# Performance work log

Hardware: AMD Instinct MI355X
Metric: run time of the kernel (lower is better)

## Reference

```python
import jax, jax.numpy as jnp
import numpy as np

B, C_ATT, C_VAL = 1, 64, 64
T, H, W = 40, 32, 32
HW = H * W
TOPK = 10
TEMP = 0.07
NEIGHBOR_RANGE = 24  # circle mode -> radius = 24 // 2
NON_MASK_LEN = 1     # first frame is not masked
NEG_INF = -1e30


def _spatial_neighbor_circle(h, w, neighbor_range):
    """Circle-mode spatial neighbor mask, (h*w, h*w) bool."""
    radius = neighbor_range // 2
    gy, gx = jnp.meshgrid(jnp.arange(h, dtype=jnp.float32),
                          jnp.arange(w, dtype=jnp.float32), indexing='ij')
    dy = gy[:, :, None, None] - gy[None, None, :, :]
    dx = gx[:, :, None, None] - gx[None, None, :, :]
    dist = jnp.sqrt(dy * dy + dx * dx)
    return (dist < radius).reshape(h * w, h * w)


def setup_inputs() -> dict:
    key0 = jax.random.key(0)
    k1, k2, k3 = jax.random.split(key0, 3)
    query = jax.random.normal(k1, (B, C_ATT, H, W), dtype=jnp.float32)
    key = jax.random.normal(k2, (B, C_ATT, T, H, W), dtype=jnp.float32)
    value = jax.random.normal(k3, (B, C_VAL, T, H, W), dtype=jnp.float32)
    mask = _spatial_neighbor_circle(H, W, NEIGHBOR_RANGE)  # (HW, HW) bool
    return {"query": query, "key": key, "value": value, "mask": mask}


def _l2_normalize(x, axis, eps=1e-12):
    # matches F.normalize(p=2): x / max(||x||, eps)
    n = jnp.sqrt(jnp.sum(x * x, axis=axis, keepdims=True))
    return x / jnp.maximum(n, eps)


def reference(query, key, value, mask):
    # normalize along channel dim
    q = _l2_normalize(query, axis=1).reshape(B, C_ATT, HW)          # (B,C,Q)
    k = _l2_normalize(key, axis=1).reshape(B, C_ATT, T * HW)        # (B,C,K)
    v = value.reshape(B, C_VAL, T * HW)                             # (B,Cv,K)

    # affinity over all keys vs all queries (chunking in the original is a
    # pure memory optimization; the math per query column is identical)
    aff = jnp.einsum('bck,bcq->bkq', k, q) / TEMP                   # (B,K,Q)

    # build full mask: first NON_MASK_LEN frames fully visible, remaining
    # frames restricted to the spatial-neighbor circle
    tiled = jnp.tile(mask, (T - NON_MASK_LEN, 1))                   # ((T-nm)*HW, Q)
    full_mask = jnp.concatenate(
        [jnp.ones((NON_MASK_LEN * HW, HW), dtype=bool), tiled], axis=0)  # (K,Q)
    aff = jnp.where(full_mask[None], aff, NEG_INF)

    # top-k over the key dimension, per query
    aff_qk = jnp.swapaxes(aff, 1, 2)                                # (B,Q,K)
    top_vals, top_idx = jax.lax.top_k(aff_qk, TOPK)                 # (B,Q,topk)
    weights = jax.nn.softmax(top_vals, axis=-1)                     # (B,Q,topk)

    # gather top-k values: (B,Cv,Q,topk)
    gathered = jnp.take_along_axis(v[:, :, None, :], top_idx[:, None, :, :], axis=3)
    out = jnp.einsum('bcqk,bqk->bcq', gathered, weights)            # (B,Cv,Q)
    return out.reshape(B, C_VAL, H, W)
```

## Files before the change

kernel.cpp:

```cpp
#include <hip/hip_runtime.h>
#include <hip/hip_bf16.h>
#include <float.h>

#define HWQ   1024
#define NK    40960
#define NCH   64
#define NTOP  10
#define NF0JOB 8
#define PVLEN (NF0JOB * NTOP)
#define CAPG  384
#define CAPW  16
#define R2    144
#define TOTU  23556
#define NBLK  1024
#define TSCALE 14.2857142857142857f
#define LOSCL  4.8828125e-4f

typedef _Float16 f16x8 __attribute__((ext_vector_type(8)));
typedef float    f32x4 __attribute__((ext_vector_type(4)));
typedef unsigned short us8 __attribute__((ext_vector_type(8)));
typedef unsigned long long u64;
typedef unsigned int       u32;

__device__ inline float bf16bits_to_f32(unsigned short u) {
    union { u32 i; float f; } z; z.i = ((u32)u) << 16; return z.f;
}
__device__ inline unsigned short f32_to_bf16bits(float x) {
    __hip_bfloat16 b = __float2bfloat16(x);
    return *(unsigned short*)&b;
}

__device__ inline int sniff_fp32(const unsigned short* __restrict__ raw) {
    const int lane = threadIdx.x & 63;
    const int e = (raw[lane] >> 7) & 0xFF;
    const u64 m = __ballot(e < 100 || e > 133);
    return __popcll(m) > 16;
}

__device__ inline u32 ord32(float v) {
    const u32 b = __float_as_uint(v);
    return b ^ (u32)(((int)b >> 31) | (int)0x80000000);
}
__device__ inline u64 pack_vi(float val, int kidx) {
    return ((u64)ord32(val) << 16) | (u32)(0xFFFF - kidx);
}
__device__ inline float unpack_val(u64 p) {
    const u32 u = (u32)(p >> 16);
    const u32 b = u ^ (~((u32)((int)u >> 31)) | 0x80000000u);
    return __uint_as_float(b);
}
__device__ inline int unpack_idx(u64 p) { return 0xFFFF - (int)(p & 0xFFFF); }

__device__ inline void ins10(u64* v, u64 pk) {
#pragma unroll
    for (int j = NTOP - 1; j >= 1; --j) {
        const bool gj = pk > v[j];
        const bool gp = pk > v[j - 1];
        v[j] = gj ? (gp ? v[j - 1] : pk) : v[j];
    }
    if (pk > v[0]) v[0] = pk;
}

__global__ __launch_bounds__(256) void prep_all(
    const void* __restrict__ qin_, const void* __restrict__ kin_,
    const void* __restrict__ vin_,
    f16x8* __restrict__ kh, f16x8* __restrict__ kl,
    f16x8* __restrict__ qh, f16x8* __restrict__ ql,
    unsigned short* __restrict__ vt, int* __restrict__ cnt)
{
    __shared__ float ssq[4][64];
    const int isf  = sniff_fp32((const unsigned short*)kin_);
    const int bid  = blockIdx.x;
    const int tid  = threadIdx.x;
    const int w    = tid >> 6;
    const int lane = tid & 63;
    const int c0   = w * 16;

    if (bid == 655) {
        cnt[tid * 4 + 0] = 0; cnt[tid * 4 + 1] = 0;
        cnt[tid * 4 + 2] = 0; cnt[tid * 4 + 3] = 0;
    }

    if (bid < 640) {
        const int key = bid * 64 + lane;
        float x[16];
        if (isf) {
            const float* p = (const float*)kin_;
#pragma unroll
            for (int i = 0; i < 16; ++i) x[i] = p[(c0 + i) * NK + key];
        } else {
            const __hip_bfloat16* p = (const __hip_bfloat16*)kin_;
#pragma unroll
            for (int i = 0; i < 16; ++i) x[i] = __bfloat162float(p[(c0 + i) * NK + key]);
        }
        float s = 0.f;
#pragma unroll
        for (int i = 0; i < 16; ++i) s = fmaf(x[i], x[i], s);
        ssq[w][lane] = s;
        __syncthreads();
        s = ssq[0][lane] + ssq[1][lane] + ssq[2][lane] + ssq[3][lane];
        const float rn = 1.0f / fmaxf(sqrtf(s), 1e-12f);

        const int tb = (key >> 4) * 128 + (key & 15);
#pragma unroll
        for (int b2 = 0; b2 < 2; ++b2) {
            f16x8 h, l;
#pragma unroll
            for (int jj = 0; jj < 8; ++jj) {
                const float xv = x[b2 * 8 + jj] * rn;
                const _Float16 hh = (_Float16)xv;
                h[jj] = hh;
                l[jj] = (_Float16)((xv - (float)hh) * 2048.0f);
            }
            kh[tb + (w * 2 + b2) * 16] = h;
            kl[tb + (w * 2 + b2) * 16] = l;
        }

        unsigned short vv[16];
        if (isf) {
            const float* p = (const float*)vin_;
#pragma unroll
            for (int i = 0; i < 16; ++i) vv[i] = f32_to_bf16bits(p[(c0 + i) * NK + key]);
        } else {
            const unsigned short* p = (const unsigned short*)vin_;
#pragma unroll
            for (int i = 0; i < 16; ++i) vv[i] = p[(c0 + i) * NK + key];
        }
        us8* dst = (us8*)(vt + (size_t)key * NCH + c0);
#pragma unroll
        for (int b2 = 0; b2 < 2; ++b2) {
            us8 o;
#pragma unroll
            for (int e = 0; e < 8; ++e) o[e] = vv[b2 * 8 + e];
            dst[b2] = o;
        }
    } else {
        const int q = (bid - 640) * 64 + lane;
        float x[16];
        if (isf) {
            const float* p = (const float*)qin_;
#pragma unroll
            for (int i = 0; i < 16; ++i) x[i] = p[(c0 + i) * HWQ + q];
        } else {
            const __hip_bfloat16* p = (const __hip_bfloat16*)qin_;
#pragma unroll
            for (int i = 0; i < 16; ++i) x[i] = __bfloat162float(p[(c0 + i) * HWQ + q]);
        }
        float s = 0.f;
#pragma unroll
        for (int i = 0; i < 16; ++i) s = fmaf(x[i], x[i], s);
        ssq[w][lane] = s;
        __syncthreads();
        s = ssq[0][lane] + ssq[1][lane] + ssq[2][lane] + ssq[3][lane];
        const float rn = 1.0f / fmaxf(sqrtf(s), 1e-12f);

        const int tb = (q >> 4) * 128 + (q & 15);
#pragma unroll
        for (int b2 = 0; b2 < 2; ++b2) {
            f16x8 h, l;
#pragma unroll
            for (int jj = 0; jj < 8; ++jj) {
                const float xv = x[b2 * 8 + jj] * rn;
                const _Float16 hh = (_Float16)xv;
                h[jj] = hh;
                l[jj] = (_Float16)((xv - (float)hh) * 2048.0f);
            }
            qh[tb + (w * 2 + b2) * 16] = h;
            ql[tb + (w * 2 + b2) * 16] = l;
        }
    }
}

__device__ inline void quad_merge_store(
    u64 (*sm)[16][NTOP], int lane, u64* out10)
{
    int p0 = 0, p1 = 0, p2 = 0, p3 = 0;
#pragma unroll
    for (int r = 0; r < NTOP; ++r) {
        const u64 h0 = sm[0][lane][p0], h1 = sm[1][lane][p1];
        const u64 h2 = sm[2][lane][p2], h3 = sm[3][lane][p3];
        u64 m = h0; int sel = 0;
        if (h1 > m) { m = h1; sel = 1; }
        if (h2 > m) { m = h2; sel = 2; }
        if (h3 > m) { m = h3; sel = 3; }
        out10[r] = m;
        p0 += (sel == 0); p1 += (sel == 1); p2 += (sel == 2); p3 += (sel == 3);
    }
}

__global__ __launch_bounds__(128) void attn_f0(
    const f16x8* __restrict__ kh, const f16x8* __restrict__ kl,
    const f16x8* __restrict__ qh, const f16x8* __restrict__ ql,
    u64* __restrict__ pv)
{
    __shared__ u64 sm[2][4][16][NTOP];

    const int tid  = threadIdx.x;
    const int w    = tid >> 6;
    const int lane = tid & 63;
    const int quad = lane >> 4;
    const int n    = lane & 15;

    const int t   = blockIdx.x * 2 + w;
    const int job = blockIdx.y;

    const int qb = t * 128 + n;
    const f16x8 bh0 = qh[qb + quad * 16];
    const f16x8 bh1 = qh[qb + (4 + quad) * 16];
    const f16x8 bl0 = ql[qb + quad * 16];
    const f16x8 bl1 = ql[qb + (4 + quad) * 16];

    u64 v[NTOP];
#pragma unroll
    for (int jj = 0; jj < NTOP; ++jj) v[jj] = 0ull;

    const int start = job * 8, end = start + 8;
    const int loff = (n + quad * 16) * 16;
    const char* ph = (const char*)kh + (size_t)start * 2048 + loff;
    const char* pl = (const char*)kl + (size_t)start * 2048 + loff;

    for (int kt = start; kt < end; ++kt) {
        const f16x8 Ah0 = *(const f16x8*)(ph);
        const f16x8 Ah1 = *(const f16x8*)(ph + 1024);
        const f16x8 Al0 = *(const f16x8*)(pl);
        const f16x8 Al1 = *(const f16x8*)(pl + 1024);

        f32x4 accH = {0.f,0.f,0.f,0.f}, accL0 = {0.f,0.f,0.f,0.f}, accL1 = {0.f,0.f,0.f,0.f};
        accH  = __builtin_amdgcn_mfma_f32_16x16x32_f16(Ah0, bh0, accH, 0, 0, 0);
        accH  = __builtin_amdgcn_mfma_f32_16x16x32_f16(Ah1, bh1, accH, 0, 0, 0);
        accL0 = __builtin_amdgcn_mfma_f32_16x16x32_f16(Ah0, bl0, accL0, 0, 0, 0);
        accL0 = __builtin_amdgcn_mfma_f32_16x16x32_f16(Al0, bh0, accL0, 0, 0, 0);
        accL1 = __builtin_amdgcn_mfma_f32_16x16x32_f16(Ah1, bl1, accL1, 0, 0, 0);
        accL1 = __builtin_amdgcn_mfma_f32_16x16x32_f16(Al1, bh1, accL1, 0, 0, 0);

        const int key0 = kt * 16 + quad * 4;
#pragma unroll
        for (int r = 0; r < 4; ++r) {
            const float val = fmaf(accL0[r] + accL1[r], LOSCL, accH[r]);
            const u64 pk = pack_vi(val, key0 + r);
            if (pk > v[NTOP - 1]) ins10(v, pk);
        }
        ph += 2048; pl += 2048;
    }

#pragma unroll
    for (int jj = 0; jj < NTOP; ++jj) sm[w][quad][n][jj] = v[jj];
    __syncthreads();

    if (lane < 16) {
        u64 out10[NTOP];
        quad_merge_store(sm[w], lane, out10);
        const int q = t * 16 + lane;
#pragma unroll
        for (int r = 0; r < NTOP; ++r) pv[(size_t)q * PVLEN + job * NTOP + r] = out10[r];
    }
}

__global__ __launch_bounds__(256) void theta_refine(
    const u64* __restrict__ pv, float* __restrict__ thmax)
{
    const int q    = blockIdx.x * 4 + (threadIdx.x >> 6);
    const int lane = threadIdx.x & 63;

    u64 l0 = pv[(size_t)q * PVLEN + lane];
    u64 l1 = (lane < 16) ? pv[(size_t)q * PVLEN + 64 + lane] : 0ull;

    u64 m = 0ull;
#pragma unroll
    for (int r = 0; r < NTOP; ++r) {
        u64 c = l0 > l1 ? l0 : l1;
#pragma unroll
        for (int off = 32; off >= 1; off >>= 1) {
            const u32 lo = (u32)c, hi = (u32)(c >> 32);
            const u32 lo2 = (u32)__shfl_xor((int)lo, off);
            const u32 hi2 = (u32)__shfl_xor((int)hi, off);
            const u64 o = ((u64)hi2 << 32) | lo2;
            if (o > c) c = o;
        }
        if (l0 == c) l0 = 0ull;
        if (l1 == c) l1 = 0ull;
        m = c;
    }
    if (lane == 0) thmax[q] = unpack_val(m);
}

__global__ __launch_bounds__(256, 4) void attn_masked(
    const f16x8* __restrict__ kh, const f16x8* __restrict__ kl,
    const f16x8* __restrict__ qh, const f16x8* __restrict__ ql,
    const float* __restrict__ thmax,
    u64* __restrict__ gcand, int* __restrict__ cnt)
{
    __shared__ u64 wcand[4][32][CAPW];
    __shared__ int wcnt[4][32];

    const int tid  = threadIdx.x;
    const int w    = tid >> 6;
    const int lane = tid & 63;
    const int quad = lane >> 4;
    const int n    = lane & 15;

    if (lane < 32) wcnt[w][lane] = 0;

    const int bidx = ((int)blockIdx.x & 7) * (NBLK / 8) + ((int)blockIdx.x >> 3);
    const int wid  = bidx * 4 + w;
    const int u0   = (int)(((long long)wid * TOTU) >> 12);
    const int u1   = (int)(((long long)(wid + 1) * TOTU) >> 12);

    f16x8 b0h0, b0h1, b0l0, b0l1, b1h0, b1h1, b1l0, b1l1;
    float theta0 = 0.f, theta1 = 0.f;
    int cur_qy = -1, q0 = 0;

    for (int u = u0; u < u1; ++u) {
        const int fm1 = u / 604;
        const int rem = u - fm1 * 604;
        int qy, off;
        if (rem < 210) {
            int t = (int)((sqrtf((float)(529 + 8 * rem)) - 23.0f) * 0.5f);
            while ((t * (t + 23)) / 2 > rem) --t;
            while (((t + 1) * (t + 24)) / 2 <= rem) ++t;
            qy = t; off = rem - (t * (t + 23)) / 2;
        } else if (rem < 417) {
            qy = 12 + (rem - 210) / 23; off = (rem - 210) % 23;
        } else {
            const int s = 603 - rem;
            int t = (int)((sqrtf((float)(529 + 8 * s)) - 23.0f) * 0.5f);
            while ((t * (t + 23)) / 2 > s) --t;
            while (((t + 1) * (t + 24)) / 2 <= s) ++t;
            qy = 31 - t;
            off = (12 + t) - 1 - (s - (t * (t + 23)) / 2);
        }
        const int rlo = (qy > 11) ? qy - 11 : 0;
        const int row = rlo + off;
        const int frame = fm1 + 1;

        if (qy != cur_qy) {
            if (cur_qy >= 0) {
                __builtin_amdgcn_wave_barrier();
                if (lane < 32) {
                    const int rc = min(wcnt[w][lane], CAPW);
                    if (rc > 0) {
                        const int qq = cur_qy * 32 + lane;
                        const int base = atomicAdd(&cnt[qq], rc);
                        for (int jf = 0; jf < rc; ++jf) {
                            const int pos = base + jf;
                            if (pos < CAPG) gcand[(size_t)qq * CAPG + pos] = wcand[w][lane][jf];
                        }
                    }
                    wcnt[w][lane] = 0;
                }
                __builtin_amdgcn_wave_barrier();
            }
            cur_qy = qy;
            const int qb = qy * 256 + n;
            b0h0 = qh[qb + quad * 16];       b0h1 = qh[qb + (4 + quad) * 16];
            b0l0 = ql[qb + quad * 16];       b0l1 = ql[qb + (4 + quad) * 16];
            b1h0 = qh[qb + 128 + quad * 16]; b1h1 = qh[qb + 128 + (4 + quad) * 16];
            b1l0 = ql[qb + 128 + quad * 16]; b1l1 = ql[qb + 128 + (4 + quad) * 16];
            q0 = qy * 32 + n;
            theta0 = thmax[q0];
            theta1 = thmax[q0 + 16];
        }

        const int dy    = row - qy;
        const int rem2  = R2 - dy * dy;
        const int tbase = frame * 64 + row * 2;
        const int keyrow = frame * 1024 + row * 32;

#pragma unroll
        for (int kt2 = 0; kt2 < 2; ++kt2) {
            const f16x8* pA = kh + (tbase + kt2) * 128 + n;
            const f16x8* pL = kl + (tbase + kt2) * 128 + n;
            const f16x8 ah0 = pA[quad * 16];
            const f16x8 ah1 = pA[(4 + quad) * 16];
            const f16x8 al0 = pL[quad * 16];
            const f16x8 al1 = pL[(4 + quad) * 16];

            f32x4 H0 = {0.f,0.f,0.f,0.f}, L00 = {0.f,0.f,0.f,0.f}, L01 = {0.f,0.f,0.f,0.f};
            f32x4 H1 = {0.f,0.f,0.f,0.f}, L10 = {0.f,0.f,0.f,0.f}, L11 = {0.f,0.f,0.f,0.f};
            H0  = __builtin_amdgcn_mfma_f32_16x16x32_f16(ah0, b0h0, H0, 0, 0, 0);
            H0  = __builtin_amdgcn_mfma_f32_16x16x32_f16(ah1, b0h1, H0, 0, 0, 0);
            L00 = __builtin_amdgcn_mfma_f32_16x16x32_f16(ah0, b0l0, L00, 0, 0, 0);
            L00 = __builtin_amdgcn_mfma_f32_16x16x32_f16(al0, b0h0, L00, 0, 0, 0);
            L01 = __builtin_amdgcn_mfma_f32_16x16x32_f16(ah1, b0l1, L01, 0, 0, 0);
            L01 = __builtin_amdgcn_mfma_f32_16x16x32_f16(al1, b0h1, L01, 0, 0, 0);
            H1  = __builtin_amdgcn_mfma_f32_16x16x32_f16(ah0, b1h0, H1, 0, 0, 0);
            H1  = __builtin_amdgcn_mfma_f32_16x16x32_f16(ah1, b1h1, H1, 0, 0, 0);
            L10 = __builtin_amdgcn_mfma_f32_16x16x32_f16(ah0, b1l0, L10, 0, 0, 0);
            L10 = __builtin_amdgcn_mfma_f32_16x16x32_f16(al0, b1h0, L10, 0, 0, 0);
            L11 = __builtin_amdgcn_mfma_f32_16x16x32_f16(ah1, b1l1, L11, 0, 0, 0);
            L11 = __builtin_amdgcn_mfma_f32_16x16x32_f16(al1, b1h1, L11, 0, 0, 0);

            const int kx0  = kt2 * 16 + quad * 4;
            const int key0 = keyrow + kx0;
#pragma unroll
            for (int r = 0; r < 4; ++r) {
                const float v0 = fmaf(L00[r] + L01[r], LOSCL, H0[r]);
                const float v1 = fmaf(L10[r] + L11[r], LOSCL, H1[r]);
                if (v0 > theta0) {
                    const int dx = kx0 + r - n;
                    if (dx * dx < rem2) {
                        const int pos = atomicAdd(&wcnt[w][n], 1);
                        if (pos < CAPW) wcand[w][n][pos] = pack_vi(v0, key0 + r);
                    }
                }
                if (v1 > theta1) {
                    const int dx = kx0 + r - 16 - n;
                    if (dx * dx < rem2) {
                        const int pos = atomicAdd(&wcnt[w][16 + n], 1);
                        if (pos < CAPW) wcand[w][16 + n][pos] = pack_vi(v1, key0 + r);
                    }
                }
            }
        }
    }

    __builtin_amdgcn_wave_barrier();
    if (cur_qy >= 0 && lane < 32) {
        const int rc = min(wcnt[w][lane], CAPW);
        if (rc > 0) {
            const int qq = cur_qy * 32 + lane;
            const int base = atomicAdd(&cnt[qq], rc);
            for (int jf = 0; jf < rc; ++jf) {
                const int pos = base + jf;
                if (pos < CAPG) gcand[(size_t)qq * CAPG + pos] = wcand[w][lane][jf];
            }
        }
    }
}

__global__ __launch_bounds__(64) void finalize_kernel(
    const u64* __restrict__ pv, const u64* __restrict__ gcand,
    const int* __restrict__ cnt, const unsigned short* __restrict__ vt,
    const unsigned short* __restrict__ kin_raw, void* __restrict__ out_)
{
    const int isf  = sniff_fp32(kin_raw);
    const int q    = blockIdx.x;
    const int lane = threadIdx.x;

    u64 lv[8];
    lv[0] = pv[(size_t)q * PVLEN + lane];
    lv[1] = (lane < 16) ? pv[(size_t)q * PVLEN + 64 + lane] : 0ull;
    const int c = min(cnt[q], CAPG);
#pragma unroll
    for (int e = 0; e < 6; ++e) {
        const int idx = e * 64 + lane;
        lv[2 + e] = (idx < c) ? gcand[(size_t)q * CAPG + idx] : 0ull;
    }

    float wv[NTOP]; int wi[NTOP];
#pragma unroll
    for (int r = 0; r < NTOP; ++r) {
        u64 m = lv[0];
#pragma unroll
        for (int e = 1; e < 8; ++e) if (lv[e] > m) m = lv[e];
#pragma unroll
        for (int off = 32; off >= 1; off >>= 1) {
            const u32 lo = (u32)m, hi = (u32)(m >> 32);
            const u32 lo2 = (u32)__shfl_xor((int)lo, off);
            const u32 hi2 = (u32)__shfl_xor((int)hi, off);
            const u64 o = ((u64)hi2 << 32) | lo2;
            if (o > m) m = o;
        }
#pragma unroll
        for (int e = 0; e < 8; ++e) if (lv[e] == m) lv[e] = 0ull;
        wv[r] = unpack_val(m); wi[r] = unpack_idx(m);
    }

    float ww[NTOP]; float wsum = 0.f;
#pragma unroll
    for (int r = 0; r < NTOP; ++r) { ww[r] = expf((wv[r] - wv[0]) * TSCALE); wsum += ww[r]; }
    const float inv = 1.0f / wsum;

    float acc = 0.f;
#pragma unroll
    for (int r = 0; r < NTOP; ++r)
        acc += ww[r] * bf16bits_to_f32(vt[(size_t)wi[r] * NCH + lane]);
    const float res = acc * inv;

    if (isf) ((float*)out_)[lane * HWQ + q] = res;
    else     ((__hip_bfloat16*)out_)[lane * HWQ + q] = __float2bfloat16(res);
}

extern "C" void kernel_launch(void* const* d_in, const int* in_sizes, int n_in,
                              void* d_out, int out_size, void* d_ws, size_t ws_size,
                              hipStream_t stream)
{
    const void* qin = d_in[0];
    const void* kin = d_in[1];
    const void* vin = d_in[2];

    char* w = (char*)d_ws;
    f16x8*          kh    = (f16x8*)(w);
    f16x8*          kl    = (f16x8*)(w + 5242880);
    f16x8*          qhv   = (f16x8*)(w + 10485760);
    f16x8*          qlv   = (f16x8*)(w + 10616832);
    unsigned short* vt    = (unsigned short*)(w + 10747904);
    u64*            pv    = (u64*)(w + 15990784);
    u64*            gcand = (u64*)(w + 16646144);
    float*          thmax = (float*)(w + 19791872);
    int*            cnt   = (int*)(w + 19795968);

    prep_all<<<656, 256, 0, stream>>>(qin, kin, vin, kh, kl, qhv, qlv, vt, cnt);
    attn_f0<<<dim3(32, 8), 128, 0, stream>>>(kh, kl, qhv, qlv, pv);
    theta_refine<<<256, 256, 0, stream>>>(pv, thmax);
    attn_masked<<<NBLK, 256, 0, stream>>>(kh, kl, qhv, qlv, thmax, gcand, cnt);
    finalize_kernel<<<HWQ, 64, 0, stream>>>(pv, gcand, cnt, vt,
                                            (const unsigned short*)kin, d_out);
}
```

Before: 121.0 us.

## Screen masked keys with high-half fp16 only, rescore candidates exactly in finalize

The masked-frame scoring pass now uses only the high fp16 half of the split q/k representation (4 MFMAs instead of 12 per tile). It compares against a threshold lowered by a fixed margin and records only key indices. The finalize kernel recomputes exact hi+lo dot products for each surviving candidate with a wave reduction before top-k selection. This cuts MFMA work and key loads in the dominant kernel. In exchange the margin admits more candidates, finalize does a serial loop per candidate, and correctness depends on the margin covering the low-half error and on CAPW/CAPG not overflowing.

```diff
diff --git a/kernel.cpp b/kernel.cpp
--- a/kernel.cpp
+++ b/kernel.cpp
@@ -15,6 +15,7 @@
 #define NBLK  1024
 #define TSCALE 14.2857142857142857f
 #define LOSCL  4.8828125e-4f
+#define MARGIN 0.004f
 
 typedef _Float16 f16x8 __attribute__((ext_vector_type(8)));
 typedef float    f32x4 __attribute__((ext_vector_type(4)));
@@ -285,12 +286,12 @@
 }
 
 __global__ __launch_bounds__(256, 4) void attn_masked(
-    const f16x8* __restrict__ kh, const f16x8* __restrict__ kl,
-    const f16x8* __restrict__ qh, const f16x8* __restrict__ ql,
+    const f16x8* __restrict__ kh,
+    const f16x8* __restrict__ qh,
     const float* __restrict__ thmax,
-    u64* __restrict__ gcand, int* __restrict__ cnt)
-{
-    __shared__ u64 wcand[4][32][CAPW];
+    u32* __restrict__ gcand, int* __restrict__ cnt)
+{
+    __shared__ u32 wcand[4][32][CAPW];
     __shared__ int wcnt[4][32];
 
     const int tid  = threadIdx.x;
@@ -306,8 +307,8 @@
     const int u0   = (int)(((long long)wid * TOTU) >> 12);
     const int u1   = (int)(((long long)(wid + 1) * TOTU) >> 12);
 
-    f16x8 b0h0, b0h1, b0l0, b0l1, b1h0, b1h1, b1l0, b1l1;
-    float theta0 = 0.f, theta1 = 0.f;
+    f16x8 b0h0, b0h1, b1h0, b1h1;
+    float thm0 = 0.f, thm1 = 0.f;
     int cur_qy = -1, q0 = 0;
 
     for (int u = u0; u < u1; ++u) {
@@ -353,12 +354,10 @@
             cur_qy = qy;
             const int qb = qy * 256 + n;
             b0h0 = qh[qb + quad * 16];       b0h1 = qh[qb + (4 + quad) * 16];
-            b0l0 = ql[qb + quad * 16];       b0l1 = ql[qb + (4 + quad) * 16];
             b1h0 = qh[qb + 128 + quad * 16]; b1h1 = qh[qb + 128 + (4 + quad) * 16];
-            b1l0 = ql[qb + 128 + quad * 16]; b1l1 = ql[qb + 128 + (4 + quad) * 16];
             q0 = qy * 32 + n;
-            theta0 = thmax[q0];
-            theta1 = thmax[q0 + 16];
+            thm0 = thmax[q0] - MARGIN;
+            thm1 = thmax[q0 + 16] - MARGIN;
         }
 
         const int dy    = row - qy;
@@ -369,45 +368,31 @@
 #pragma unroll
         for (int kt2 = 0; kt2 < 2; ++kt2) {
             const f16x8* pA = kh + (tbase + kt2) * 128 + n;
-            const f16x8* pL = kl + (tbase + kt2) * 128 + n;
             const f16x8 ah0 = pA[quad * 16];
             const f16x8 ah1 = pA[(4 + quad) * 16];
-            const f16x8 al0 = pL[quad * 16];
-            const f16x8 al1 = pL[(4 + quad) * 16];
-
-            f32x4 H0 = {0.f,0.f,0.f,0.f}, L00 = {0.f,0.f,0.f,0.f}, L01 = {0.f,0.f,0.f,0.f};
-            f32x4 H1 = {0.f,0.f,0.f,0.f}, L10 = {0.f,0.f,0.f,0.f}, L11 = {0.f,0.f,0.f,0.f};
-            H0  = __builtin_amdgcn_mfma_f32_16x16x32_f16(ah0, b0h0, H0, 0, 0, 0);
-            H0  = __builtin_amdgcn_mfma_f32_16x16x32_f16(ah1, b0h1, H0, 0, 0, 0);
-            L00 = __builtin_amdgcn_mfma_f32_16x16x32_f16(ah0, b0l0, L00, 0, 0, 0);
-            L00 = __builtin_amdgcn_mfma_f32_16x16x32_f16(al0, b0h0, L00, 0, 0, 0);
-            L01 = __builtin_amdgcn_mfma_f32_16x16x32_f16(ah1, b0l1, L01, 0, 0, 0);
-            L01 = __builtin_amdgcn_mfma_f32_16x16x32_f16(al1, b0h1, L01, 0, 0, 0);
-            H1  = __builtin_amdgcn_mfma_f32_16x16x32_f16(ah0, b1h0, H1, 0, 0, 0);
-            H1  = __builtin_amdgcn_mfma_f32_16x16x32_f16(ah1, b1h1, H1, 0, 0, 0);
-            L10 = __builtin_amdgcn_mfma_f32_16x16x32_f16(ah0, b1l0, L10, 0, 0, 0);
-            L10 = __builtin_amdgcn_mfma_f32_16x16x32_f16(al0, b1h0, L10, 0, 0, 0);
-            L11 = __builtin_amdgcn_mfma_f32_16x16x32_f16(ah1, b1l1, L11, 0, 0, 0);
-            L11 = __builtin_amdgcn_mfma_f32_16x16x32_f16(al1, b1h1, L11, 0, 0, 0);
+
+            f32x4 H0 = {0.f,0.f,0.f,0.f}, H1 = {0.f,0.f,0.f,0.f};
+            H0 = __builtin_amdgcn_mfma_f32_16x16x32_f16(ah0, b0h0, H0, 0, 0, 0);
+            H0 = __builtin_amdgcn_mfma_f32_16x16x32_f16(ah1, b0h1, H0, 0, 0, 0);
+            H1 = __builtin_amdgcn_mfma_f32_16x16x32_f16(ah0, b1h0, H1, 0, 0, 0);
+            H1 = __builtin_amdgcn_mfma_f32_16x16x32_f16(ah1, b1h1, H1, 0, 0, 0);
 
             const int kx0  = kt2 * 16 + quad * 4;
             const int key0 = keyrow + kx0;
 #pragma unroll
             for (int r = 0; r < 4; ++r) {
-                const float v0 = fmaf(L00[r] + L01[r], LOSCL, H0[r]);
-                const float v1 = fmaf(L10[r] + L11[r], LOSCL, H1[r]);
-                if (v0 > theta0) {
+                if (H0[r] > thm0) {
                     const int dx = kx0 + r - n;
                     if (dx * dx < rem2) {
                         const int pos = atomicAdd(&wcnt[w][n], 1);
-                        if (pos < CAPW) wcand[w][n][pos] = pack_vi(v0, key0 + r);
+                        if (pos < CAPW) wcand[w][n][pos] = (u32)(key0 + r);
                     }
                 }
-                if (v1 > theta1) {
+                if (H1[r] > thm1) {
                     const int dx = kx0 + r - 16 - n;
                     if (dx * dx < rem2) {
                         const int pos = atomicAdd(&wcnt[w][16 + n], 1);
-                        if (pos < CAPW) wcand[w][16 + n][pos] = pack_vi(v1, key0 + r);
+                        if (pos < CAPW) wcand[w][16 + n][pos] = (u32)(key0 + r);
                     }
                 }
             }
@@ -429,22 +414,38 @@
 }
 
 __global__ __launch_bounds__(64) void finalize_kernel(
-    const u64* __restrict__ pv, const u64* __restrict__ gcand,
-    const int* __restrict__ cnt, const unsigned short* __restrict__ vt,
+    const u64* __restrict__ pv, const u32* __restrict__ gcand,
+    const int* __restrict__ cnt,
+    const f16x8* __restrict__ kh, const f16x8* __restrict__ kl,
+    const f16x8* __restrict__ qh, const f16x8* __restrict__ ql,
+    const unsigned short* __restrict__ vt,
     const unsigned short* __restrict__ kin_raw, void* __restrict__ out_)
 {
     const int isf  = sniff_fp32(kin_raw);
     const int q    = blockIdx.x;
     const int lane = threadIdx.x;
 
+    const int qfrag = (q >> 4) * 128 + (lane >> 3) * 16 + (q & 15);
+    const float qf = (float)qh[qfrag][lane & 7]
+                   + (float)ql[qfrag][lane & 7] * LOSCL;
+
     u64 lv[8];
     lv[0] = pv[(size_t)q * PVLEN + lane];
     lv[1] = (lane < 16) ? pv[(size_t)q * PVLEN + 64 + lane] : 0ull;
+#pragma unroll
+    for (int e = 2; e < 8; ++e) lv[e] = 0ull;
+
     const int c = min(cnt[q], CAPG);
-#pragma unroll
-    for (int e = 0; e < 6; ++e) {
-        const int idx = e * 64 + lane;
-        lv[2 + e] = (idx < c) ? gcand[(size_t)q * CAPG + idx] : 0ull;
+    for (int e = 0; e < c; ++e) {
+        const int k = (int)gcand[(size_t)q * CAPG + e];
+        const int kfrag = (k >> 4) * 128 + (lane >> 3) * 16 + (k & 15);
+        const float kf = (float)kh[kfrag][lane & 7]
+                       + (float)kl[kfrag][lane & 7] * LOSCL;
+        float part = qf * kf;
+#pragma unroll
+        for (int off = 32; off >= 1; off >>= 1) part += __shfl_xor(part, off);
+        const u64 pk = pack_vi(part, k);
+        if ((e & 63) == lane) lv[2 + (e >> 6)] = pk;
     }
 
     float wv[NTOP]; int wi[NTOP];
@@ -496,14 +497,14 @@
     f16x8*          qlv   = (f16x8*)(w + 10616832);
     unsigned short* vt    = (unsigned short*)(w + 10747904);
     u64*            pv    = (u64*)(w + 15990784);
-    u64*            gcand = (u64*)(w + 16646144);
-    float*          thmax = (float*)(w + 19791872);
-    int*            cnt   = (int*)(w + 19795968);
+    u32*            gcand = (u32*)(w + 16646144);
+    float*          thmax = (float*)(w + 18219008);
+    int*            cnt   = (int*)(w + 18223104);
 
     prep_all<<<656, 256, 0, stream>>>(qin, kin, vin, kh, kl, qhv, qlv, vt, cnt);
     attn_f0<<<dim3(32, 8), 128, 0, stream>>>(kh, kl, qhv, qlv, pv);
     theta_refine<<<256, 256, 0, stream>>>(pv, thmax);
-    attn_masked<<<NBLK, 256, 0, stream>>>(kh, kl, qhv, qlv, thmax, gcand, cnt);
-    finalize_kernel<<<HWQ, 64, 0, stream>>>(pv, gcand, cnt, vt,
-                                            (const unsigned short*)kin, d_out);
-}
+    attn_masked<<<NBLK, 256, 0, stream>>>(kh, qhv, thmax, gcand, cnt);
+    finalize_kernel<<<HWQ, 64, 0, stream>>>(pv, gcand, cnt, kh, kl, qhv, qlv,
+                                            vt, (const unsigned short*)kin, d_out);
+}
```

Result: slower. 271.4 us (+124.4%).
